# Kernel optimization log

Measured on AMD Instinct MI355X. Metric: run time of the kernel, lower is better.

The kernel has to match this reference:

```python
import jax, jax.numpy as jnp
import numpy as np

NUM_MODELS = 64
OUT_F = 256
IN_F = 256
B = 32768
F0 = 2
F1 = 2


def setup_inputs() -> dict:
    key = jax.random.key(0)
    k1, k2, k3, k4 = jax.random.split(key, 4)
    sqrt_k = float(np.sqrt(1.0 / NUM_MODELS))
    weights = 2 * sqrt_k * jax.random.uniform(k1, (NUM_MODELS, OUT_F, IN_F), dtype=jnp.float32) - sqrt_k
    biases = 2 * sqrt_k * jax.random.uniform(k2, (NUM_MODELS, OUT_F), dtype=jnp.float32) - sqrt_k
    inputs = jax.random.normal(k3, (B, IN_F // F1), dtype=jnp.float32)
    indices = jax.random.randint(k4, (B,), 0, NUM_MODELS, dtype=jnp.int64)
    return {"inputs": inputs, "weights": weights, "biases": biases,
            "indices": indices, "factor0": F0, "factor1": F1}


def reference(inputs, weights, biases, indices, factor0, factor1):
    out_sub = weights.shape[1] // factor0
    in_sub = weights.shape[2] // factor1
    # Gather per-sample weight slices: (B, out_sub, in_sub)
    subweight = weights[indices, :out_sub, :in_sub]
    subbias = biases[indices, :out_sub]  # (B, out_sub)
    # Batched matvec + bias
    return jnp.einsum('boi,bi->bo', subweight, inputs) + subbias
```

## Files before the change

kernel.cpp:

```cpp
#include <hip/hip_runtime.h>
#include <hip/hip_bf16.h>

#define NMODELS 64
#define NB      32768
#define INF     256
#define OUTF    256
#define INS     128
#define OUTS    128
#define TILE_M  64
#define NT      10
#define NHB     128
#define WCONV_BLOCKS 512

typedef unsigned int u32;
typedef unsigned short u16;
using bf16x8  = __attribute__((ext_vector_type(8))) short;
using f32x4   = __attribute__((ext_vector_type(4))) float;
using float4v = __attribute__((ext_vector_type(4))) float;
using short8v = __attribute__((ext_vector_type(8))) short;

__device__ __forceinline__ u16 f2bf(float f) {
    union { float fv; u32 u; } v; v.fv = f;
    u32 u = v.u;
    u += 0x7fffu + ((u >> 16) & 1u);
    return (u16)(u >> 16);
}

__device__ __forceinline__ void async_copy16(const void* g, void* l) {
    __builtin_amdgcn_global_load_lds((const __attribute__((address_space(1))) u32*)g,
                                     (__attribute__((address_space(3))) u32*)l,
                                     16, 0, 0);
}

__global__ __launch_bounds__(256) void k_prep(const int* __restrict__ idx,
                                              const float* __restrict__ w,
                                              int* __restrict__ hist_part,
                                              u16* __restrict__ wb) {
    const int t = threadIdx.x;
    const int b = blockIdx.x;
    if (b < WCONV_BLOCKS) {
        const int cid = b * 256 + t;
        const int m   = cid >> 11;
        const int rem = cid & 2047;
        const int row = rem >> 4;
        const int c   = rem & 15;
        const float* src = w + ((size_t)m * OUTF + row) * INF + c * 8;
        float4v v0 = *(const float4v*)(src);
        float4v v1 = *(const float4v*)(src + 4);
        short8v s;
        s[0]=(short)f2bf(v0.x); s[1]=(short)f2bf(v0.y); s[2]=(short)f2bf(v0.z); s[3]=(short)f2bf(v0.w);
        s[4]=(short)f2bf(v1.x); s[5]=(short)f2bf(v1.y); s[6]=(short)f2bf(v1.z); s[7]=(short)f2bf(v1.w);
        *(short8v*)(wb + ((size_t)(m * 128 + row) * 128) + ((c ^ (row & 15)) * 8)) = s;
    } else {
        __shared__ int h[NMODELS];
        const int b2 = b - WCONV_BLOCKS;
        if (t < NMODELS) h[t] = 0;
        __syncthreads();
        atomicAdd(&h[idx[b2 * 256 + t]], 1);
        __syncthreads();
        if (t < NMODELS) hist_part[b2 * NMODELS + t] = h[t];
    }
}

__global__ __launch_bounds__(256) void k_scatter(const int* __restrict__ idx,
                                                 const int* __restrict__ hist_part,
                                                 int* __restrict__ starts_g,
                                                 int* __restrict__ counts_g,
                                                 int* __restrict__ perm) {
    __shared__ int H[NHB * NMODELS];
    __shared__ int starts_s[NMODELS];
    __shared__ int pre_s[NMODELS];
    __shared__ int lh[NMODELS];
    const int t = threadIdx.x;
    const int b = blockIdx.x;
    #pragma unroll
    for (int k = 0; k < (NHB * NMODELS) / 256; ++k)
        H[k * 256 + t] = hist_part[k * 256 + t];
    if (t < NMODELS) lh[t] = 0;
    __syncthreads();
    if (t < NMODELS) {
        int sum = 0, pre = 0;
        for (int bb = 0; bb < NHB; ++bb) {
            if (bb == b) pre = sum;
            sum += H[bb * NMODELS + t];
        }
        pre_s[t] = pre;
        int x = sum;
        #pragma unroll
        for (int d = 1; d < 64; d <<= 1) {
            int y = __shfl_up(x, d, 64);
            if (t >= d) x += y;
        }
        starts_s[t] = x - sum;
        if (b == 0) { starts_g[t] = x - sum; counts_g[t] = sum; }
    }
    __syncthreads();
    const int i = b * 256 + t;
    const int m = idx[i];
    const int r = atomicAdd(&lh[m], 1);
    perm[starts_s[m] + pre_s[m] + r] = i;
}

__global__ __launch_bounds__(256) void k_gemm(const float* __restrict__ x,
                                              const u16* __restrict__ wb,
                                              const float* __restrict__ bias,
                                              const int* __restrict__ starts_g,
                                              const int* __restrict__ counts_g,
                                              const int* __restrict__ perm,
                                              float* __restrict__ out) {
    __shared__ __align__(16) u16 Ws[OUTS * 128];
    const int m   = blockIdx.x;
    const int cnt = counts_g[m];
    if ((int)blockIdx.y * TILE_M >= cnt) return;
    const int start = starts_g[m];
    const int t    = threadIdx.x;
    const int wave = t >> 6;
    const int lane = t & 63;
    const int quad = lane >> 4;
    const int lr   = lane & 15;

    {
        const char* g = (const char*)(wb + (size_t)m * (OUTS * 128));
        char* l = (char*)Ws;
        #pragma unroll
        for (int itc = 0; itc < 8; ++itc) {
            const int off = itc * 4096 + wave * 1024;
            async_copy16(g + off + lane * 16, l + off);
        }
    }
    float bv[8];
    #pragma unroll
    for (int nt = 0; nt < 8; ++nt) bv[nt] = bias[m * OUTF + nt * 16 + lr];

    int xoff[4];
    #pragma unroll
    for (int k0 = 0; k0 < 4; ++k0) xoff[k0] = ((k0 * 4 + quad) ^ lr) * 8;
    const int rowbase = lr * 128;

    __syncthreads();

    for (int tile = blockIdx.y; tile * TILE_M < cnt; tile += NT) {
        const int row0 = tile * TILE_M + wave * 16;
        int p = -1;
        if (row0 + lr < cnt) p = perm[start + row0 + lr];
        const int gx = (p >= 0) ? p : 0;
        const float* xr = x + (size_t)gx * INS + quad * 8;
        f32x4 xa[8];
        #pragma unroll
        for (int k0 = 0; k0 < 4; ++k0) {
            xa[2 * k0]     = *(const float4v*)(xr + k0 * 32);
            xa[2 * k0 + 1] = *(const float4v*)(xr + k0 * 32 + 4);
        }
        bf16x8 afr[4];
        #pragma unroll
        for (int k0 = 0; k0 < 4; ++k0) {
            bf16x8 a;
            a[0] = (short)f2bf(xa[2*k0].x); a[1] = (short)f2bf(xa[2*k0].y);
            a[2] = (short)f2bf(xa[2*k0].z); a[3] = (short)f2bf(xa[2*k0].w);
            a[4] = (short)f2bf(xa[2*k0+1].x); a[5] = (short)f2bf(xa[2*k0+1].y);
            a[6] = (short)f2bf(xa[2*k0+1].z); a[7] = (short)f2bf(xa[2*k0+1].w);
            afr[k0] = a;
        }
        f32x4 acc[8];
        #pragma unroll
        for (int nt = 0; nt < 8; ++nt) acc[nt] = (f32x4){0.f, 0.f, 0.f, 0.f};
        #pragma unroll
        for (int k0 = 0; k0 < 4; ++k0) {
            #pragma unroll
            for (int nt = 0; nt < 8; ++nt) {
                bf16x8 bfr = *(const bf16x8*)&Ws[nt * 2048 + rowbase + xoff[k0]];
                acc[nt] = __builtin_amdgcn_mfma_f32_16x16x32_bf16(afr[k0], bfr, acc[nt], 0, 0, 0);
            }
        }
        #pragma unroll
        for (int r = 0; r < 4; ++r) {
            const int g = __shfl(p, quad * 4 + r, 64);
            if (g >= 0) {
                float* orow = out + (size_t)g * OUTS;
                #pragma unroll
                for (int nt = 0; nt < 8; ++nt)
                    orow[nt * 16 + lr] = acc[nt][r] + bv[nt];
            }
        }
    }
}

extern "C" void kernel_launch(void* const* d_in, const int* in_sizes, int n_in,
                              void* d_out, int out_size, void* d_ws, size_t ws_size,
                              hipStream_t stream) {
    const float* x    = (const float*)d_in[0];
    const float* w    = (const float*)d_in[1];
    const float* bias = (const float*)d_in[2];
    const int*   idx  = (const int*)d_in[3];
    float* out = (float*)d_out;

    int* ws        = (int*)d_ws;
    int* hist_part = ws;
    int* starts_g  = ws + 8192;
    int* counts_g  = ws + 8256;
    int* perm      = ws + 8320;
    u16* wb        = (u16*)(ws + 8320 + 32768);

    k_prep   <<<dim3(WCONV_BLOCKS + NHB), dim3(256), 0, stream>>>(idx, w, hist_part, wb);
    k_scatter<<<dim3(NHB),                dim3(256), 0, stream>>>(idx, hist_part, starts_g, counts_g, perm);
    k_gemm   <<<dim3(NMODELS, NT),        dim3(256), 0, stream>>>(x, wb, bias, starts_g, counts_g, perm, out);
}
```

Baseline: 96.05 us.

## Replace histogram+scan with fixed-capacity bins via global atomics and prefetch next tile

```diff
diff --git a/kernel.cpp b/kernel.cpp
--- a/kernel.cpp
+++ b/kernel.cpp
@@ -9,7 +9,8 @@
 #define OUTS    128
 #define TILE_M  64
 #define NT      10
-#define NHB     128
+#define BINCAP  1024
+#define NSB     128
 #define WCONV_BLOCKS 512
 
 typedef unsigned int u32;
@@ -32,14 +33,27 @@
                                      16, 0, 0);
 }
 
-__global__ __launch_bounds__(256) void k_prep(const int* __restrict__ idx,
-                                              const float* __restrict__ w,
-                                              int* __restrict__ hist_part,
-                                              u16* __restrict__ wb) {
+__global__ __launch_bounds__(256) void k_scatconv(const int* __restrict__ idx,
+                                                  const float* __restrict__ w,
+                                                  int* __restrict__ cursors,
+                                                  int* __restrict__ perm,
+                                                  u16* __restrict__ wb) {
     const int t = threadIdx.x;
     const int b = blockIdx.x;
-    if (b < WCONV_BLOCKS) {
-        const int cid = b * 256 + t;
+    if (b < NSB) {
+        __shared__ int h[NMODELS];
+        __shared__ int base[NMODELS];
+        if (t < NMODELS) h[t] = 0;
+        __syncthreads();
+        const int i = b * 256 + t;
+        const int m = idx[i];
+        const int r = atomicAdd(&h[m], 1);
+        __syncthreads();
+        if (t < NMODELS && h[t] != 0) base[t] = atomicAdd(&cursors[t], h[t]);
+        __syncthreads();
+        perm[(m << 10) + base[m] + r] = i;
+    } else {
+        const int cid = (b - NSB) * 256 + t;
         const int m   = cid >> 11;
         const int rem = cid & 2047;
         const int row = rem >> 4;
@@ -51,68 +65,19 @@
         s[0]=(short)f2bf(v0.x); s[1]=(short)f2bf(v0.y); s[2]=(short)f2bf(v0.z); s[3]=(short)f2bf(v0.w);
         s[4]=(short)f2bf(v1.x); s[5]=(short)f2bf(v1.y); s[6]=(short)f2bf(v1.z); s[7]=(short)f2bf(v1.w);
         *(short8v*)(wb + ((size_t)(m * 128 + row) * 128) + ((c ^ (row & 15)) * 8)) = s;
-    } else {
-        __shared__ int h[NMODELS];
-        const int b2 = b - WCONV_BLOCKS;
-        if (t < NMODELS) h[t] = 0;
-        __syncthreads();
-        atomicAdd(&h[idx[b2 * 256 + t]], 1);
-        __syncthreads();
-        if (t < NMODELS) hist_part[b2 * NMODELS + t] = h[t];
     }
-}
-
-__global__ __launch_bounds__(256) void k_scatter(const int* __restrict__ idx,
-                                                 const int* __restrict__ hist_part,
-                                                 int* __restrict__ starts_g,
-                                                 int* __restrict__ counts_g,
-                                                 int* __restrict__ perm) {
-    __shared__ int H[NHB * NMODELS];
-    __shared__ int starts_s[NMODELS];
-    __shared__ int pre_s[NMODELS];
-    __shared__ int lh[NMODELS];
-    const int t = threadIdx.x;
-    const int b = blockIdx.x;
-    #pragma unroll
-    for (int k = 0; k < (NHB * NMODELS) / 256; ++k)
-        H[k * 256 + t] = hist_part[k * 256 + t];
-    if (t < NMODELS) lh[t] = 0;
-    __syncthreads();
-    if (t < NMODELS) {
-        int sum = 0, pre = 0;
-        for (int bb = 0; bb < NHB; ++bb) {
-            if (bb == b) pre = sum;
-            sum += H[bb * NMODELS + t];
-        }
-        pre_s[t] = pre;
-        int x = sum;
-        #pragma unroll
-        for (int d = 1; d < 64; d <<= 1) {
-            int y = __shfl_up(x, d, 64);
-            if (t >= d) x += y;
-        }
-        starts_s[t] = x - sum;
-        if (b == 0) { starts_g[t] = x - sum; counts_g[t] = sum; }
-    }
-    __syncthreads();
-    const int i = b * 256 + t;
-    const int m = idx[i];
-    const int r = atomicAdd(&lh[m], 1);
-    perm[starts_s[m] + pre_s[m] + r] = i;
 }
 
 __global__ __launch_bounds__(256) void k_gemm(const float* __restrict__ x,
                                               const u16* __restrict__ wb,
                                               const float* __restrict__ bias,
-                                              const int* __restrict__ starts_g,
-                                              const int* __restrict__ counts_g,
+                                              const int* __restrict__ cursors,
                                               const int* __restrict__ perm,
                                               float* __restrict__ out) {
     __shared__ __align__(16) u16 Ws[OUTS * 128];
     const int m   = blockIdx.x;
-    const int cnt = counts_g[m];
+    const int cnt = cursors[m];
     if ((int)blockIdx.y * TILE_M >= cnt) return;
-    const int start = starts_g[m];
     const int t    = threadIdx.x;
     const int wave = t >> 6;
     const int lane = t & 63;
@@ -128,38 +93,40 @@
             async_copy16(g + off + lane * 16, l + off);
         }
     }
-    float bv[8];
+    float4v bv4[8];
     #pragma unroll
-    for (int nt = 0; nt < 8; ++nt) bv[nt] = bias[m * OUTF + nt * 16 + lr];
+    for (int nt = 0; nt < 8; ++nt)
+        bv4[nt] = *(const float4v*)(bias + m * OUTF + nt * 16 + quad * 4);
 
     int xoff[4];
     #pragma unroll
     for (int k0 = 0; k0 < 4; ++k0) xoff[k0] = ((k0 * 4 + quad) ^ lr) * 8;
     const int rowbase = lr * 128;
+    const int pbase   = m << 10;
+
+    int tile = blockIdx.y;
+    int row  = tile * TILE_M + wave * 16 + lr;
+    int p    = (row < cnt) ? perm[pbase + row] : -1;
+    const float* xr = x + (size_t)((p < 0) ? 0 : p) * INS + quad * 8;
+    float4v xa[8];
+    #pragma unroll
+    for (int k0 = 0; k0 < 4; ++k0) {
+        xa[2 * k0]     = *(const float4v*)(xr + k0 * 32);
+        xa[2 * k0 + 1] = *(const float4v*)(xr + k0 * 32 + 4);
+    }
 
     __syncthreads();
 
-    for (int tile = blockIdx.y; tile * TILE_M < cnt; tile += NT) {
-        const int row0 = tile * TILE_M + wave * 16;
-        int p = -1;
-        if (row0 + lr < cnt) p = perm[start + row0 + lr];
-        const int gx = (p >= 0) ? p : 0;
-        const float* xr = x + (size_t)gx * INS + quad * 8;
-        f32x4 xa[8];
-        #pragma unroll
-        for (int k0 = 0; k0 < 4; ++k0) {
-            xa[2 * k0]     = *(const float4v*)(xr + k0 * 32);
-            xa[2 * k0 + 1] = *(const float4v*)(xr + k0 * 32 + 4);
-        }
-        bf16x8 afr[4];
+    for (;;) {
+        bf16x8 xb[4];
         #pragma unroll
         for (int k0 = 0; k0 < 4; ++k0) {
             bf16x8 a;
-            a[0] = (short)f2bf(xa[2*k0].x); a[1] = (short)f2bf(xa[2*k0].y);
-            a[2] = (short)f2bf(xa[2*k0].z); a[3] = (short)f2bf(xa[2*k0].w);
+            a[0] = (short)f2bf(xa[2*k0].x);   a[1] = (short)f2bf(xa[2*k0].y);
+            a[2] = (short)f2bf(xa[2*k0].z);   a[3] = (short)f2bf(xa[2*k0].w);
             a[4] = (short)f2bf(xa[2*k0+1].x); a[5] = (short)f2bf(xa[2*k0+1].y);
             a[6] = (short)f2bf(xa[2*k0+1].z); a[7] = (short)f2bf(xa[2*k0+1].w);
-            afr[k0] = a;
+            xb[k0] = a;
         }
         f32x4 acc[8];
         #pragma unroll
@@ -168,20 +135,31 @@
         for (int k0 = 0; k0 < 4; ++k0) {
             #pragma unroll
             for (int nt = 0; nt < 8; ++nt) {
-                bf16x8 bfr = *(const bf16x8*)&Ws[nt * 2048 + rowbase + xoff[k0]];
-                acc[nt] = __builtin_amdgcn_mfma_f32_16x16x32_bf16(afr[k0], bfr, acc[nt], 0, 0, 0);
+                bf16x8 wfr = *(const bf16x8*)&Ws[nt * 2048 + rowbase + xoff[k0]];
+                acc[nt] = __builtin_amdgcn_mfma_f32_16x16x32_bf16(wfr, xb[k0], acc[nt], 0, 0, 0);
             }
         }
-        #pragma unroll
-        for (int r = 0; r < 4; ++r) {
-            const int g = __shfl(p, quad * 4 + r, 64);
-            if (g >= 0) {
-                float* orow = out + (size_t)g * OUTS;
-                #pragma unroll
-                for (int nt = 0; nt < 8; ++nt)
-                    orow[nt * 16 + lr] = acc[nt][r] + bv[nt];
+        const int curp = p;
+        const int ntile = tile + NT;
+        const bool more = (ntile * TILE_M < cnt);
+        if (more) {
+            row = ntile * TILE_M + wave * 16 + lr;
+            p   = (row < cnt) ? perm[pbase + row] : -1;
+            const float* xr2 = x + (size_t)((p < 0) ? 0 : p) * INS + quad * 8;
+            #pragma unroll
+            for (int k0 = 0; k0 < 4; ++k0) {
+                xa[2 * k0]     = *(const float4v*)(xr2 + k0 * 32);
+                xa[2 * k0 + 1] = *(const float4v*)(xr2 + k0 * 32 + 4);
             }
         }
+        if (curp >= 0) {
+            float* orow = out + (size_t)curp * OUTS + quad * 4;
+            #pragma unroll
+            for (int nt = 0; nt < 8; ++nt)
+                *(float4v*)(orow + nt * 16) = acc[nt] + bv4[nt];
+        }
+        if (!more) break;
+        tile = ntile;
     }
 }
 
@@ -194,14 +172,12 @@
     const int*   idx  = (const int*)d_in[3];
     float* out = (float*)d_out;
 
-    int* ws        = (int*)d_ws;
-    int* hist_part = ws;
-    int* starts_g  = ws + 8192;
-    int* counts_g  = ws + 8256;
-    int* perm      = ws + 8320;
-    u16* wb        = (u16*)(ws + 8320 + 32768);
+    int* ws      = (int*)d_ws;
+    int* cursors = ws;
+    int* perm    = ws + 64;
+    u16* wb      = (u16*)(ws + 64 + 65536);
 
-    k_prep   <<<dim3(WCONV_BLOCKS + NHB), dim3(256), 0, stream>>>(idx, w, hist_part, wb);
-    k_scatter<<<dim3(NHB),                dim3(256), 0, stream>>>(idx, hist_part, starts_g, counts_g, perm);
-    k_gemm   <<<dim3(NMODELS, NT),        dim3(256), 0, stream>>>(x, wb, bias, starts_g, counts_g, perm, out);
+    hipMemsetAsync(cursors, 0, NMODELS * sizeof(int), stream);
+    k_scatconv<<<dim3(NSB + WCONV_BLOCKS), dim3(256), 0, stream>>>(idx, w, cursors, perm, wb);
+    k_gemm    <<<dim3(NMODELS, NT),        dim3(256), 0, stream>>>(x, wb, bias, cursors, perm, out);
 }
```

Measured after the change: 94.83 us. Within noise of the previous version (-1.3%).
